# Kernel tuning notes

Measured on AMD Instinct MI355X. Metric: run time of the kernel, lower is better.

Reference implementation:

```python
import jax, jax.numpy as jnp
import numpy as np

B, T_LAT = 64, 1024
K, PAD = 15, 7
# SMPL-style parents for 24 joints (joint 0 = root)
PARENTS = [0, 0, 0, 0, 1, 2, 3, 4, 5, 6, 7, 8, 9, 9, 9, 12, 13, 14, 16, 17, 18, 19, 20, 21]


def _fine_adjacency():
    # edges of the kinematic tree; +1 virtual root-displacement node (Aberman find_neighbor, dist=1)
    edges = [(PARENTS[j], j) for j in range(1, 24)]  # 23 edges
    n = len(edges) + 1  # 24 graph nodes
    A = np.eye(n, dtype=bool)
    for i, (pi, ci) in enumerate(edges):
        for j, (pj, cj) in enumerate(edges):
            if {pi, ci} & {pj, cj}:
                A[i, j] = True
        if pi == 0 or ci == 0:  # edges touching the root neighbor the virtual root node
            A[i, n - 1] = A[n - 1, i] = True
    return A


def _coarsen(A, pools):
    m = len(pools)
    Ac = np.eye(m, dtype=bool)
    for a in range(m):
        for b in range(m):
            if A[np.ix_(pools[a], pools[b])].any():
                Ac[a, b] = True
    return Ac


def _unpool_weight(pools, n_fine, cpj):
    # SkeletonUnpool: binary matrix copying each coarse joint's channels to its fine members
    W = np.zeros((n_fine * cpj, len(pools) * cpj), np.float32)
    for i, grp in enumerate(pools):
        for j in grp:
            for c in range(cpj):
                W[j * cpj + c, i * cpj + c] = 1.0
    return W


def _conv_mask(A, in_cpj, out_cpj, k):
    n = A.shape[0]
    M = np.zeros((n * out_cpj, n * in_cpj, k), np.float32)
    for a in range(n):
        for b in range(n):
            if A[a, b]:
                M[a * out_cpj:(a + 1) * out_cpj, b * in_cpj:(b + 1) * in_cpj, :] = 1.0
    return M


def _lin_mask(A, in_cpj, out_cpj):
    n = A.shape[0]
    M = np.zeros((n * out_cpj, n * in_cpj), np.float32)
    for a in range(n):
        for b in range(n):
            if A[a, b]:
                M[a * out_cpj:(a + 1) * out_cpj, b * in_cpj:(b + 1) * in_cpj] = 1.0
    return M


def setup_inputs() -> dict:
    key = jax.random.key(0)
    ks = jax.random.split(key, 12)
    A0 = _fine_adjacency()                           # 24 fine graph nodes
    P0 = [[2 * i, 2 * i + 1] for i in range(12)]     # pooling 24 -> 12
    P1 = [[2 * i, 2 * i + 1] for i in range(6)]      # pooling 12 -> 6
    A1 = _coarsen(A0, P0)                            # 12-node coarse adjacency

    inp = {
        'x': jax.random.normal(ks[0], (B, T_LAT, 96), jnp.float32),      # latent: 6 joints x 16 ch
        'offset0': jax.random.normal(ks[1], (B, 12, 3), jnp.float32),
        'offset1': jax.random.normal(ks[2], (B, 24, 3), jnp.float32),
        'W_unpool0': jnp.asarray(_unpool_weight(P1, 12, 16)),            # (192, 96)
        'W_unpool1': jnp.asarray(_unpool_weight(P0, 24, 8)),             # (192, 96)
        'conv_w0': jax.random.normal(ks[3], (96, 192, K), jnp.float32) * 0.05,
        'conv_b0': jax.random.normal(ks[4], (96,), jnp.float32) * 0.05,
        'conv_w1': jax.random.normal(ks[5], (96, 192, K), jnp.float32) * 0.05,
        'conv_b1': jax.random.normal(ks[6], (96,), jnp.float32) * 0.05,
        'off_w0': jax.random.normal(ks[7], (96, 36), jnp.float32) * 0.05,
        'off_b0': jax.random.normal(ks[8], (96,), jnp.float32) * 0.05,
        'off_w1': jax.random.normal(ks[9], (96, 72), jnp.float32) * 0.05,
        'off_b1': jax.random.normal(ks[10], (96,), jnp.float32) * 0.05,
        'conv_mask0': jnp.asarray(_conv_mask(A1, 16, 8, K)),
        'conv_mask1': jnp.asarray(_conv_mask(A0, 8, 4, K)),
        'off_mask0': jnp.asarray(_lin_mask(A1, 3, 8)),
        'off_mask1': jnp.asarray(_lin_mask(A0, 3, 4)),
    }
    return inp


def _upsample2(h):
    # nn.Upsample(scale_factor=2, mode='linear', align_corners=False) on last axis
    b, c, t = h.shape
    return jax.image.resize(h, (b, c, 2 * t), method='linear')


def _conv1d(h, w, b):
    y = jax.lax.conv_general_dilated(h, w, (1,), [(PAD, PAD)],
                                     dimension_numbers=('NCH', 'OIH', 'NCH'))
    return y + b[None, :, None]


def reference(x, offset0, offset1, W_unpool0, W_unpool1,
              conv_w0, conv_b0, conv_w1, conv_b1,
              off_w0, off_b0, off_w1, off_b1,
              conv_mask0, conv_mask1, off_mask0, off_mask1):
    h = jnp.swapaxes(x, -2, -1)                       # (B, C_lat, T)
    # ---- stage 0: upsample time, unpool 6->12 joints, masked conv, offset, LeakyReLU
    h = _upsample2(h)
    h = jnp.einsum('oc,bct->bot', W_unpool0, h)       # (B, 192, 2T)
    h = _conv1d(h, conv_w0 * conv_mask0, conv_b0)     # (B, 96, 2T)
    off = offset0.reshape(offset0.shape[0], -1) @ (off_w0 * off_mask0).T + off_b0
    h = h + off[:, :, None] / 100.0
    h = jax.nn.leaky_relu(h, 0.2)
    # ---- stage 1 (last layer: no activation)
    h = _upsample2(h)
    h = jnp.einsum('oc,bct->bot', W_unpool1, h)       # (B, 192, 4T)
    h = _conv1d(h, conv_w1 * conv_mask1, conv_b1)     # (B, 96, 4T)
    off = offset1.reshape(offset1.shape[0], -1) @ (off_w1 * off_mask1).T + off_b1
    h = h + off[:, :, None] / 100.0
    return h[:, :, :-1]                               # trim last frame
```

## Files before the change

### kernel.cpp

```cpp
#include <hip/hip_runtime.h>

typedef unsigned short ushort_t;
typedef unsigned int u32;
typedef short bf16x8 __attribute__((ext_vector_type(8)));
typedef float f32x4 __attribute__((ext_vector_type(4)));
typedef u32 u32x4 __attribute__((ext_vector_type(4)));

__device__ __forceinline__ float bf2f(ushort_t u) {
    u32 x = ((u32)u) << 16; float f; __builtin_memcpy(&f, &x, 4); return f;
}
__device__ __forceinline__ ushort_t f2bf(float f) {
    u32 x; __builtin_memcpy(&x, &f, 4);
    x = x + 0x7fffu + ((x >> 16) & 1u);
    return (ushort_t)(x >> 16);
}

#define NBB 128
#define UROWS 136
#define USTRB 208
#define UB_BYTES (UROWS * USTRB)
#define LDS_TOTAL UB_BYTES
#define LSTR1 261

__global__ void prepA(const float* __restrict__ w0, const float* __restrict__ m0,
                      const float* __restrict__ w1, const float* __restrict__ m1,
                      const float* __restrict__ offw0, const float* __restrict__ offb0,
                      const float* __restrict__ omask0, const float* __restrict__ convb0,
                      const float* __restrict__ off0,
                      const float* __restrict__ offw1, const float* __restrict__ offb1,
                      const float* __restrict__ omask1, const float* __restrict__ convb1,
                      const float* __restrict__ off1,
                      float* __restrict__ Wplain, float* __restrict__ ADD0,
                      float* __restrict__ ADD1)
{
    int idx = blockIdx.x * 256 + threadIdx.x;
    if (idx < 18432) {
        int o = idx % 96;
        int cc = (idx / 96) % 96;
        int st = idx / 9216;
        const float* w = st ? w1 : w0;
        const float* mk = st ? m1 : m0;
        int cpj = st ? 8 : 16;
        int i = cc / cpj, c = cc % cpj;
        float s[15];
#pragma unroll
        for (int k = 0; k < 15; ++k) s[k] = 0.f;
#pragma unroll
        for (int d = 0; d < 2; ++d) {
            int f = (2 * i + d) * cpj + c;
            int base = (o * 192 + f) * 15;
#pragma unroll
            for (int k = 0; k < 15; ++k)
                s[k] += w[base + k] * mk[base + k];
        }
#pragma unroll
        for (int k = 0; k < 15; ++k)
            Wplain[st * 138240 + (k * 96 + cc) * 96 + o] = s[k];
    } else if (idx < 18432 + 12288) {
        int a = idx - 18432;
        int st = a / 6144; int a2 = a % 6144;
        int o = a2 % 96, b = a2 / 96;
        const float* ow = st ? offw1 : offw0;
        const float* ob = st ? offb1 : offb0;
        const float* om = st ? omask1 : omask0;
        const float* cb = st ? convb1 : convb0;
        const float* of = st ? off1 : off0;
        int J = st ? 72 : 36;
        float s = 0.f;
        for (int j2 = 0; j2 < J; ++j2) s += ow[o * J + j2] * om[o * J + j2] * of[b * J + j2];
        (st ? ADD1 : ADD0)[b * 96 + o] = cb[o] + (s + ob[o]) * 0.01f;
    }
}

__global__ void prepB(const float* __restrict__ Wplain,
                      ushort_t* __restrict__ Wp0, ushort_t* __restrict__ Wp1)
{
    int idx = blockIdx.x * 256 + threadIdx.x;
    if (idx >= 331776) return;
    int o = idx % 96; int t = idx / 96;
    int cc = t % 96; t /= 96;
    int j = t % 9; t /= 9;
    int p = t % 2; int st = t / 2;
    const float* WP = Wplain + (size_t)st * 138240;
    int kk[4]; float cf[4];
    if (p == 0) { kk[0]=2*j;   cf[0]=0.75f; kk[1]=2*j-2; cf[1]=0.25f;
                  kk[2]=2*j+1; cf[2]=0.25f; kk[3]=2*j-1; cf[3]=0.75f; }
    else        { kk[0]=2*j;   cf[0]=0.25f; kk[1]=2*j-2; cf[1]=0.75f;
                  kk[2]=2*j-1; cf[2]=0.75f; kk[3]=2*j-3; cf[3]=0.25f; }
    float s = 0.f;
#pragma unroll
    for (int q = 0; q < 4; ++q) {
        int k = kk[q];
        if (k >= 0 && k < 15) s += cf[q] * WP[(k * 96 + cc) * 96 + o];
    }
    int lane = (o & 15) | (((cc >> 3) & 3) << 4);
    int mh = (o >> 4) / 3, m = (o >> 4) % 3;
    int pos = ((((j * 2 + mh) * 2 + p) * 9) + (cc >> 5) * 3 + m) * 512 + lane * 8 + (cc & 7);
    (st ? Wp1 : Wp0)[pos] = f2bf(s);
}

template<int BF16SRC>
__global__ void prep_G(const float* __restrict__ WP, const float* __restrict__ srcF,
                       const ushort_t* __restrict__ srcB, float* __restrict__ G, int T)
{
    int idx = blockIdx.x * 256 + threadIdx.x;
    if (idx >= 184320) return;
    int o = idx % 96; int t = idx / 96;
    int k = t % 15; t /= 15;
    int side = t % 2; int b = t / 2;
    const float* wk = WP + (size_t)k * 9216 + o;
    int row = side ? T - 1 : 0;
    float s = 0.f;
    if (BF16SRC) {
        const ushort_t* xr = srcB + ((size_t)b * T + row) * 96;
        for (int cc = 0; cc < 96; ++cc)
            s += wk[cc * 96] * bf2f(xr[cc]);
    } else {
        const float* xr = srcF + ((size_t)b * T + row) * 96;
        for (int cc = 0; cc < 96; ++cc)
            s += wk[cc * 96] * bf2f(f2bf(xr[cc]));
    }
    G[((size_t)(b * 96 + o) * 15 + k) * 2 + side] = s;
}

__global__ void prep_cfb(const float* __restrict__ G, float* __restrict__ CF,
                         float* __restrict__ CB)
{
    int idx = blockIdx.x * 256 + threadIdx.x;
    if (idx >= 86016) return;
    int seg = idx % 14; int r = idx / 14;
    int o = r % 96; int b = r / 96;
    bool front = seg < 7; int t = front ? seg : seg - 7;
    float s = 0.f;
    if (front) { for (int k = 0; k <= 6 - t; ++k)   s += G[(((size_t)(b*96+o)*15)+k)*2 + 0]; }
    else       { for (int k = 14 - t; k <= 14; ++k) s += G[(((size_t)(b*96+o)*15)+k)*2 + 1]; }
    (front ? CF : CB)[(b * 7 + t) * 96 + o] = s;
}

template<int STAGE>
__launch_bounds__(256, 4)
__global__ void conv_poly(const float* __restrict__ Xf, const ushort_t* __restrict__ Hbf,
                          const ushort_t* __restrict__ Wp, const float* __restrict__ ADD,
                          const float* __restrict__ CF, const float* __restrict__ CB,
                          ushort_t* __restrict__ Hout, float* __restrict__ Fout, int T)
{
    extern __shared__ char smem[];
    char* Ub = smem;

    const int tid = threadIdx.x;
    const int lane = tid & 63;
    const int wid = tid >> 6;
    const int b = blockIdx.y;
    const int tg = blockIdx.x;
    const int mh = blockIdx.z;
    const int phase = wid & 1;
    const int nq = wid >> 1;
    const int rb0 = tg * NBB - 4;

    const ushort_t* wgl = Wp + (size_t)(mh * 2 + phase) * 4608 + lane * 8;

    if (STAGE == 0) {
        const float* xb = Xf + (size_t)b * T * 96;
        for (int idx = tid; idx < UROWS * 12; idx += 256) {
            int r = idx / 12, q = idx - r * 12;
            int rg = rb0 + r; rg = rg < 0 ? 0 : (rg > T - 1 ? T - 1 : rg);
            const float* src = xb + (size_t)rg * 96 + q * 8;
            float4 a = *(const float4*)src;
            float4 c2 = *(const float4*)(src + 4);
            u32x4 v;
            v[0] = (u32)f2bf(a.x) | ((u32)f2bf(a.y) << 16);
            v[1] = (u32)f2bf(a.z) | ((u32)f2bf(a.w) << 16);
            v[2] = (u32)f2bf(c2.x) | ((u32)f2bf(c2.y) << 16);
            v[3] = (u32)f2bf(c2.z) | ((u32)f2bf(c2.w) << 16);
            *(u32x4*)(Ub + r * USTRB + q * 16) = v;
        }
    } else {
        const ushort_t* xb = Hbf + (size_t)b * T * 96;
        for (int idx = tid; idx < UROWS * 12; idx += 256) {
            int r = idx / 12, q = idx - r * 12;
            int rg = rb0 + r; rg = rg < 0 ? 0 : (rg > T - 1 ? T - 1 : rg);
            u32x4 v = *(const u32x4*)(xb + (size_t)rg * 96 + q * 8);
            *(u32x4*)(Ub + r * USTRB + q * 16) = v;
        }
    }
    __syncthreads();

    f32x4 acc[3][4];
#pragma unroll
    for (int m = 0; m < 3; ++m)
#pragma unroll
        for (int n = 0; n < 4; ++n) acc[m][n] = (f32x4){0.f, 0.f, 0.f, 0.f};

    const int rowbase = 64 * nq + (lane & 15);
    const int og16 = (lane >> 4) * 16;

#pragma unroll
    for (int j = 0; j < 9; ++j) {
        const ushort_t* wj = wgl + (size_t)j * 18432;
        bf16x8 aj[9];
#pragma unroll
        for (int q = 0; q < 9; ++q)
            aj[q] = *(const bf16x8*)(wj + q * 512);

        const int bj = (rowbase + j) * USTRB;
#pragma unroll
        for (int cb = 0; cb < 3; ++cb) {
            const int off0 = bj + cb * 64 + og16;
            bf16x8 bfr[4];
#pragma unroll
            for (int n = 0; n < 4; ++n)
                bfr[n] = *(const bf16x8*)(Ub + off0 + n * 16 * USTRB);
#pragma unroll
            for (int m = 0; m < 3; ++m)
#pragma unroll
                for (int n = 0; n < 4; ++n)
                    acc[m][n] = __builtin_amdgcn_mfma_f32_16x16x32_bf16(aj[cb * 3 + m], bfr[n], acc[m][n], 0, 0, 0);
        }
    }

    const int T2 = 2 * T;
    const int t0 = tg * 2 * NBB;
    const int og4 = (lane >> 4) * 4;

    __syncthreads();

    if (STAGE == 0) {
        ushort_t* L0 = (ushort_t*)Ub;
#pragma unroll
        for (int m = 0; m < 3; ++m) {
            int obase = mh * 48 + m * 16 + og4;
            float addv[4];
#pragma unroll
            for (int rr = 0; rr < 4; ++rr) addv[rr] = ADD[b * 96 + obase + rr];
#pragma unroll
            for (int n = 0; n < 4; ++n) {
                int tl = 2 * (rowbase + 16 * n) + phase;
                int tgl = t0 + tl;
                ushort_t pk[4];
#pragma unroll
                for (int rr = 0; rr < 4; ++rr) {
                    float v = acc[m][n][rr] + addv[rr];
                    if (tgl < 7)                   v -= CF[(b * 7 + tgl) * 96 + obase + rr];
                    if (tgl >= T2 - 7 && tgl < T2) v -= CB[(b * 7 + tgl - (T2 - 7)) * 96 + obase + rr];
                    v = v > 0.f ? v : 0.2f * v;
                    pk[rr] = f2bf(v);
                }
                uint2 w2;
                w2.x = (u32)pk[0] | ((u32)pk[1] << 16);
                w2.y = (u32)pk[2] | ((u32)pk[3] << 16);
                *(uint2*)((char*)L0 + tl * 104 + (m * 16 + og4) * 2) = w2;
            }
        }
        __syncthreads();
        for (int g = tid; g < 256 * 6; g += 256) {
            int row = g / 6, col = g % 6;
            int t = t0 + row;
            if (t < T2) {
                u32x4 v = *(const u32x4*)((char*)L0 + row * 104 + col * 16);
                *(u32x4*)((char*)Hout + ((size_t)(b * T2 + t) * 96 + mh * 48) * 2 + col * 16) = v;
            }
        }
    } else {
        const int TO = T2 - 1;
        float* L1 = (float*)Ub;
#pragma unroll
        for (int m = 0; m < 3; ++m) {
            int obase = mh * 48 + m * 16 + og4;
            float addv[4];
#pragma unroll
            for (int rr = 0; rr < 4; ++rr) addv[rr] = ADD[b * 96 + obase + rr];
#pragma unroll
            for (int n = 0; n < 4; ++n) {
                int tl = 2 * (rowbase + 16 * n) + phase;
                int tgl = t0 + tl;
#pragma unroll
                for (int rr = 0; rr < 4; ++rr) {
                    float v = acc[m][n][rr] + addv[rr];
                    if (tgl < 7)                   v -= CF[(b * 7 + tgl) * 96 + obase + rr];
                    if (tgl >= T2 - 7 && tgl < T2) v -= CB[(b * 7 + tgl - (T2 - 7)) * 96 + obase + rr];
                    L1[(og4 + rr) * LSTR1 + tl] = v;
                }
            }
            __syncthreads();
            for (int g = tid; g < 4096; g += 256) {
                int row = g >> 8, col = g & 255;
                int t = t0 + col;
                if (t < TO) {
                    int o_g = mh * 48 + m * 16 + row;
                    Fout[((size_t)(b * 96 + o_g)) * TO + t] = L1[row * LSTR1 + col];
                }
            }
            __syncthreads();
        }
    }
}

extern "C" void kernel_launch(void* const* d_in, const int* in_sizes, int n_in,
                              void* d_out, int out_size, void* d_ws, size_t ws_size,
                              hipStream_t stream)
{
    const float* x       = (const float*)d_in[0];
    const float* offset0 = (const float*)d_in[1];
    const float* offset1 = (const float*)d_in[2];
    const float* conv_w0 = (const float*)d_in[5];
    const float* conv_b0 = (const float*)d_in[6];
    const float* conv_w1 = (const float*)d_in[7];
    const float* conv_b1 = (const float*)d_in[8];
    const float* off_w0  = (const float*)d_in[9];
    const float* off_b0  = (const float*)d_in[10];
    const float* off_w1  = (const float*)d_in[11];
    const float* off_b1  = (const float*)d_in[12];
    const float* cmask0  = (const float*)d_in[13];
    const float* cmask1  = (const float*)d_in[14];
    const float* omask0  = (const float*)d_in[15];
    const float* omask1  = (const float*)d_in[16];

    char* ws = (char*)d_ws;
    float*    Wplain = (float*)(ws);
    ushort_t* Wp0    = (ushort_t*)(ws + 1105920);
    ushort_t* Wp1    = (ushort_t*)(ws + 1437696);
    float*    ADD0   = (float*)(ws + 1769472);
    float*    ADD1   = (float*)(ws + 1794048);
    float*    CF0    = (float*)(ws + 1818624);
    float*    CB0    = (float*)(ws + 1990656);
    float*    CF1    = (float*)(ws + 2162688);
    float*    CB1    = (float*)(ws + 2334720);
    float*    G0     = (float*)(ws + 2506752);
    float*    G1     = (float*)(ws + 3244032);
    ushort_t* H1     = (ushort_t*)(ws + 3981312);
    float* out = (float*)d_out;

    prepA<<<120, 256, 0, stream>>>(conv_w0, cmask0, conv_w1, cmask1,
                                   off_w0, off_b0, omask0, conv_b0, offset0,
                                   off_w1, off_b1, omask1, conv_b1, offset1,
                                   Wplain, ADD0, ADD1);
    prepB<<<1296, 256, 0, stream>>>(Wplain, Wp0, Wp1);
    prep_G<0><<<720, 256, 0, stream>>>(Wplain, x, nullptr, G0, 1024);
    prep_cfb<<<336, 256, 0, stream>>>(G0, CF0, CB0);

    conv_poly<0><<<dim3(8, 64, 2), 256, LDS_TOTAL, stream>>>(x, nullptr, Wp0, ADD0, CF0, CB0,
                                                             H1, nullptr, 1024);
    prep_G<1><<<720, 256, 0, stream>>>(Wplain + 138240, nullptr, H1, G1, 2048);
    prep_cfb<<<336, 256, 0, stream>>>(G1, CF1, CB1);
    conv_poly<1><<<dim3(16, 64, 2), 256, LDS_TOTAL, stream>>>(nullptr, H1, Wp1, ADD1, CF1, CB1,
                                                              nullptr, out, 2048);
}
```

Baseline: 127.3 us.

## Merge output-channel halves into one block, widen per-warp time tile, prefetch weights

Removes the grid z-dimension that split the 96 output channels into two blocks. Each block now computes both halves: warps split by channel half and phase, and each warp covers 128 time rows with 8 N-tiles instead of 4. The goal is to stage the input tile in LDS once instead of twice and halve the block count. Weight fragments are now loaded in three groups, with the next tap's first group prefetched. The accumulator doubles to 96 floats per lane, so launch bounds drop to 3 blocks per CU. The stage-1 LDS transpose gains a small row-dependent column shift to reduce bank conflicts, and the epilogue is serialized per channel half with extra barriers.

```diff
diff --git a/kernel.cpp b/kernel.cpp
--- a/kernel.cpp
+++ b/kernel.cpp
@@ -138,7 +138,7 @@
 }
 
 template<int STAGE>
-__launch_bounds__(256, 4)
+__launch_bounds__(256, 3)
 __global__ void conv_poly(const float* __restrict__ Xf, const ushort_t* __restrict__ Hbf,
                           const ushort_t* __restrict__ Wp, const float* __restrict__ ADD,
                           const float* __restrict__ CF, const float* __restrict__ CB,
@@ -152,12 +152,16 @@
     const int wid = tid >> 6;
     const int b = blockIdx.y;
     const int tg = blockIdx.x;
-    const int mh = blockIdx.z;
     const int phase = wid & 1;
-    const int nq = wid >> 1;
+    const int mhw = wid >> 1;
     const int rb0 = tg * NBB - 4;
 
-    const ushort_t* wgl = Wp + (size_t)(mh * 2 + phase) * 4608 + lane * 8;
+    const ushort_t* wgl = Wp + (size_t)(mhw * 2 + phase) * 4608 + lane * 8;
+
+    bf16x8 a0[3];
+#pragma unroll
+    for (int q = 0; q < 3; ++q)
+        a0[q] = *(const bf16x8*)(wgl + q * 512);
 
     if (STAGE == 0) {
         const float* xb = Xf + (size_t)b * T * 96;
@@ -185,36 +189,46 @@
     }
     __syncthreads();
 
-    f32x4 acc[3][4];
+    f32x4 acc[3][8];
 #pragma unroll
     for (int m = 0; m < 3; ++m)
 #pragma unroll
-        for (int n = 0; n < 4; ++n) acc[m][n] = (f32x4){0.f, 0.f, 0.f, 0.f};
-
-    const int rowbase = 64 * nq + (lane & 15);
+        for (int n = 0; n < 8; ++n) acc[m][n] = (f32x4){0.f, 0.f, 0.f, 0.f};
+
+    const int rowbase = lane & 15;
     const int og16 = (lane >> 4) * 16;
 
 #pragma unroll
     for (int j = 0; j < 9; ++j) {
         const ushort_t* wj = wgl + (size_t)j * 18432;
-        bf16x8 aj[9];
-#pragma unroll
-        for (int q = 0; q < 9; ++q)
-            aj[q] = *(const bf16x8*)(wj + q * 512);
-
+        bf16x8 a1[3], a2[3];
+#pragma unroll
+        for (int q = 0; q < 3; ++q) a1[q] = *(const bf16x8*)(wj + (3 + q) * 512);
+#pragma unroll
+        for (int q = 0; q < 3; ++q) a2[q] = *(const bf16x8*)(wj + (6 + q) * 512);
+        bf16x8 a0n[3];
+        if (j < 8) {
+#pragma unroll
+            for (int q = 0; q < 3; ++q) a0n[q] = *(const bf16x8*)(wj + 18432 + q * 512);
+        }
         const int bj = (rowbase + j) * USTRB;
 #pragma unroll
         for (int cb = 0; cb < 3; ++cb) {
             const int off0 = bj + cb * 64 + og16;
-            bf16x8 bfr[4];
-#pragma unroll
-            for (int n = 0; n < 4; ++n)
+            const bf16x8* af = (cb == 0) ? a0 : (cb == 1) ? a1 : a2;
+            bf16x8 bfr[8];
+#pragma unroll
+            for (int n = 0; n < 8; ++n)
                 bfr[n] = *(const bf16x8*)(Ub + off0 + n * 16 * USTRB);
 #pragma unroll
             for (int m = 0; m < 3; ++m)
 #pragma unroll
-                for (int n = 0; n < 4; ++n)
-                    acc[m][n] = __builtin_amdgcn_mfma_f32_16x16x32_bf16(aj[cb * 3 + m], bfr[n], acc[m][n], 0, 0, 0);
+                for (int n = 0; n < 8; ++n)
+                    acc[m][n] = __builtin_amdgcn_mfma_f32_16x16x32_bf16(af[m], bfr[n], acc[m][n], 0, 0, 0);
+        }
+        if (j < 8) {
+#pragma unroll
+            for (int q = 0; q < 3; ++q) a0[q] = a0n[q];
         }
     }
 
@@ -227,70 +241,82 @@
     if (STAGE == 0) {
         ushort_t* L0 = (ushort_t*)Ub;
 #pragma unroll
-        for (int m = 0; m < 3; ++m) {
-            int obase = mh * 48 + m * 16 + og4;
-            float addv[4];
-#pragma unroll
-            for (int rr = 0; rr < 4; ++rr) addv[rr] = ADD[b * 96 + obase + rr];
-#pragma unroll
-            for (int n = 0; n < 4; ++n) {
-                int tl = 2 * (rowbase + 16 * n) + phase;
-                int tgl = t0 + tl;
-                ushort_t pk[4];
-#pragma unroll
-                for (int rr = 0; rr < 4; ++rr) {
-                    float v = acc[m][n][rr] + addv[rr];
-                    if (tgl < 7)                   v -= CF[(b * 7 + tgl) * 96 + obase + rr];
-                    if (tgl >= T2 - 7 && tgl < T2) v -= CB[(b * 7 + tgl - (T2 - 7)) * 96 + obase + rr];
-                    v = v > 0.f ? v : 0.2f * v;
-                    pk[rr] = f2bf(v);
+        for (int mc = 0; mc < 2; ++mc) {
+            if (mhw == mc) {
+#pragma unroll
+                for (int m = 0; m < 3; ++m) {
+                    int obase = mc * 48 + m * 16 + og4;
+                    float addv[4];
+#pragma unroll
+                    for (int rr = 0; rr < 4; ++rr) addv[rr] = ADD[b * 96 + obase + rr];
+#pragma unroll
+                    for (int n = 0; n < 8; ++n) {
+                        int tl = 2 * (rowbase + 16 * n) + phase;
+                        int tgl = t0 + tl;
+                        ushort_t pk[4];
+#pragma unroll
+                        for (int rr = 0; rr < 4; ++rr) {
+                            float v = acc[m][n][rr] + addv[rr];
+                            if (tgl < 7)                   v -= CF[(b * 7 + tgl) * 96 + obase + rr];
+                            if (tgl >= T2 - 7 && tgl < T2) v -= CB[(b * 7 + tgl - (T2 - 7)) * 96 + obase + rr];
+                            v = v > 0.f ? v : 0.2f * v;
+                            pk[rr] = f2bf(v);
+                        }
+                        uint2 w2;
+                        w2.x = (u32)pk[0] | ((u32)pk[1] << 16);
+                        w2.y = (u32)pk[2] | ((u32)pk[3] << 16);
+                        *(uint2*)((char*)L0 + tl * 104 + (m * 16 + og4) * 2) = w2;
+                    }
                 }
-                uint2 w2;
-                w2.x = (u32)pk[0] | ((u32)pk[1] << 16);
-                w2.y = (u32)pk[2] | ((u32)pk[3] << 16);
-                *(uint2*)((char*)L0 + tl * 104 + (m * 16 + og4) * 2) = w2;
             }
-        }
-        __syncthreads();
-        for (int g = tid; g < 256 * 6; g += 256) {
-            int row = g / 6, col = g % 6;
-            int t = t0 + row;
-            if (t < T2) {
-                u32x4 v = *(const u32x4*)((char*)L0 + row * 104 + col * 16);
-                *(u32x4*)((char*)Hout + ((size_t)(b * T2 + t) * 96 + mh * 48) * 2 + col * 16) = v;
+            __syncthreads();
+            for (int g = tid; g < 256 * 6; g += 256) {
+                int row = g / 6, col = g % 6;
+                int t = t0 + row;
+                if (t < T2) {
+                    u32x4 v = *(const u32x4*)((char*)L0 + row * 104 + col * 16);
+                    *(u32x4*)((char*)Hout + ((size_t)(b * T2 + t) * 96 + mc * 48) * 2 + col * 16) = v;
+                }
             }
+            __syncthreads();
         }
     } else {
         const int TO = T2 - 1;
         float* L1 = (float*)Ub;
 #pragma unroll
-        for (int m = 0; m < 3; ++m) {
-            int obase = mh * 48 + m * 16 + og4;
-            float addv[4];
-#pragma unroll
-            for (int rr = 0; rr < 4; ++rr) addv[rr] = ADD[b * 96 + obase + rr];
-#pragma unroll
-            for (int n = 0; n < 4; ++n) {
-                int tl = 2 * (rowbase + 16 * n) + phase;
-                int tgl = t0 + tl;
-#pragma unroll
-                for (int rr = 0; rr < 4; ++rr) {
-                    float v = acc[m][n][rr] + addv[rr];
-                    if (tgl < 7)                   v -= CF[(b * 7 + tgl) * 96 + obase + rr];
-                    if (tgl >= T2 - 7 && tgl < T2) v -= CB[(b * 7 + tgl - (T2 - 7)) * 96 + obase + rr];
-                    L1[(og4 + rr) * LSTR1 + tl] = v;
+        for (int mc = 0; mc < 2; ++mc) {
+#pragma unroll
+            for (int m = 0; m < 3; ++m) {
+                if (mhw == mc) {
+                    int obase = mc * 48 + m * 16 + og4;
+                    float addv[4];
+#pragma unroll
+                    for (int rr = 0; rr < 4; ++rr) addv[rr] = ADD[b * 96 + obase + rr];
+#pragma unroll
+                    for (int n = 0; n < 8; ++n) {
+                        int tl = 2 * (rowbase + 16 * n) + phase;
+                        int tgl = t0 + tl;
+#pragma unroll
+                        for (int rr = 0; rr < 4; ++rr) {
+                            float v = acc[m][n][rr] + addv[rr];
+                            if (tgl < 7)                   v -= CF[(b * 7 + tgl) * 96 + obase + rr];
+                            if (tgl >= T2 - 7 && tgl < T2) v -= CB[(b * 7 + tgl - (T2 - 7)) * 96 + obase + rr];
+                            int rloc = og4 + rr;
+                            L1[rloc * LSTR1 + tl + ((rloc >> 2) & 1)] = v;
+                        }
+                    }
                 }
+                __syncthreads();
+                for (int g = tid; g < 4096; g += 256) {
+                    int row = g >> 8, col = g & 255;
+                    int t = t0 + col;
+                    if (t < TO) {
+                        int o_g = mc * 48 + m * 16 + row;
+                        Fout[((size_t)(b * 96 + o_g)) * TO + t] = L1[row * LSTR1 + col + ((row >> 2) & 1)];
+                    }
+                }
+                __syncthreads();
             }
-            __syncthreads();
-            for (int g = tid; g < 4096; g += 256) {
-                int row = g >> 8, col = g & 255;
-                int t = t0 + col;
-                if (t < TO) {
-                    int o_g = mh * 48 + m * 16 + row;
-                    Fout[((size_t)(b * 96 + o_g)) * TO + t] = L1[row * LSTR1 + col];
-                }
-            }
-            __syncthreads();
         }
     }
 }
@@ -338,10 +364,10 @@
     prep_G<0><<<720, 256, 0, stream>>>(Wplain, x, nullptr, G0, 1024);
     prep_cfb<<<336, 256, 0, stream>>>(G0, CF0, CB0);
 
-    conv_poly<0><<<dim3(8, 64, 2), 256, LDS_TOTAL, stream>>>(x, nullptr, Wp0, ADD0, CF0, CB0,
-                                                             H1, nullptr, 1024);
+    conv_poly<0><<<dim3(8, 64), 256, LDS_TOTAL, stream>>>(x, nullptr, Wp0, ADD0, CF0, CB0,
+                                                          H1, nullptr, 1024);
     prep_G<1><<<720, 256, 0, stream>>>(Wplain + 138240, nullptr, H1, G1, 2048);
     prep_cfb<<<336, 256, 0, stream>>>(G1, CF1, CB1);
-    conv_poly<1><<<dim3(16, 64, 2), 256, LDS_TOTAL, stream>>>(nullptr, H1, Wp1, ADD1, CF1, CB1,
-                                                              nullptr, out, 2048);
-}
+    conv_poly<1><<<dim3(16, 64), 256, LDS_TOTAL, stream>>>(nullptr, H1, Wp1, ADD1, CF1, CB1,
+                                                           nullptr, out, 2048);
+}
```

Measured after the change: 182.8 us. 1.44x slower.

## Fold boundary-correction prep kernels into conv epilogue and pipeline weight loads

Applied to the files above, without the earlier changes.

Removes the separate prep_G and prep_cfb launches and computes the front/back edge-padding corrections inside the edge tiles of each conv kernel, storing them in LDS. Weight fragments for the next tap are prefetched while the current tap's MFMAs run, replacing the bulk load of nine fragments per iteration. The fp32 epilogue transpose buffer gets a small stagger to reduce LDS bank conflicts. This cuts four kernel launches and their global round trips, at the cost of serial per-thread work in the edge blocks (up to 7×96 MACs per output) that may lengthen the tail.

```diff
diff --git a/kernel.cpp b/kernel.cpp
--- a/kernel.cpp
+++ b/kernel.cpp
@@ -19,8 +19,9 @@
 #define UROWS 136
 #define USTRB 208
 #define UB_BYTES (UROWS * USTRB)
-#define LDS_TOTAL UB_BYTES
+#define EPI_OFF 2048
 #define LSTR1 261
+#define LDS_TOTAL (EPI_OFF + 256 * 104)
 
 __global__ void prepA(const float* __restrict__ w0, const float* __restrict__ m0,
                       const float* __restrict__ w1, const float* __restrict__ m1,
@@ -99,49 +100,11 @@
     (st ? Wp1 : Wp0)[pos] = f2bf(s);
 }
 
-template<int BF16SRC>
-__global__ void prep_G(const float* __restrict__ WP, const float* __restrict__ srcF,
-                       const ushort_t* __restrict__ srcB, float* __restrict__ G, int T)
-{
-    int idx = blockIdx.x * 256 + threadIdx.x;
-    if (idx >= 184320) return;
-    int o = idx % 96; int t = idx / 96;
-    int k = t % 15; t /= 15;
-    int side = t % 2; int b = t / 2;
-    const float* wk = WP + (size_t)k * 9216 + o;
-    int row = side ? T - 1 : 0;
-    float s = 0.f;
-    if (BF16SRC) {
-        const ushort_t* xr = srcB + ((size_t)b * T + row) * 96;
-        for (int cc = 0; cc < 96; ++cc)
-            s += wk[cc * 96] * bf2f(xr[cc]);
-    } else {
-        const float* xr = srcF + ((size_t)b * T + row) * 96;
-        for (int cc = 0; cc < 96; ++cc)
-            s += wk[cc * 96] * bf2f(f2bf(xr[cc]));
-    }
-    G[((size_t)(b * 96 + o) * 15 + k) * 2 + side] = s;
-}
-
-__global__ void prep_cfb(const float* __restrict__ G, float* __restrict__ CF,
-                         float* __restrict__ CB)
-{
-    int idx = blockIdx.x * 256 + threadIdx.x;
-    if (idx >= 86016) return;
-    int seg = idx % 14; int r = idx / 14;
-    int o = r % 96; int b = r / 96;
-    bool front = seg < 7; int t = front ? seg : seg - 7;
-    float s = 0.f;
-    if (front) { for (int k = 0; k <= 6 - t; ++k)   s += G[(((size_t)(b*96+o)*15)+k)*2 + 0]; }
-    else       { for (int k = 14 - t; k <= 14; ++k) s += G[(((size_t)(b*96+o)*15)+k)*2 + 1]; }
-    (front ? CF : CB)[(b * 7 + t) * 96 + o] = s;
-}
-
 template<int STAGE>
 __launch_bounds__(256, 4)
 __global__ void conv_poly(const float* __restrict__ Xf, const ushort_t* __restrict__ Hbf,
-                          const ushort_t* __restrict__ Wp, const float* __restrict__ ADD,
-                          const float* __restrict__ CF, const float* __restrict__ CB,
+                          const ushort_t* __restrict__ Wp, const float* __restrict__ WPst,
+                          const float* __restrict__ ADD,
                           ushort_t* __restrict__ Hout, float* __restrict__ Fout, int T)
 {
     extern __shared__ char smem[];
@@ -158,6 +121,11 @@
     const int rb0 = tg * NBB - 4;
 
     const ushort_t* wgl = Wp + (size_t)(mh * 2 + phase) * 4608 + lane * 8;
+
+    bf16x8 a0[3];
+#pragma unroll
+    for (int q = 0; q < 3; ++q)
+        a0[q] = *(const bf16x8*)(wgl + q * 512);
 
     if (STAGE == 0) {
         const float* xb = Xf + (size_t)b * T * 96;
@@ -197,15 +165,21 @@
 #pragma unroll
     for (int j = 0; j < 9; ++j) {
         const ushort_t* wj = wgl + (size_t)j * 18432;
-        bf16x8 aj[9];
-#pragma unroll
-        for (int q = 0; q < 9; ++q)
-            aj[q] = *(const bf16x8*)(wj + q * 512);
-
+        bf16x8 a1[3], a2[3];
+#pragma unroll
+        for (int q = 0; q < 3; ++q) a1[q] = *(const bf16x8*)(wj + (3 + q) * 512);
+#pragma unroll
+        for (int q = 0; q < 3; ++q) a2[q] = *(const bf16x8*)(wj + (6 + q) * 512);
+        bf16x8 a0n[3];
+        if (j < 8) {
+#pragma unroll
+            for (int q = 0; q < 3; ++q) a0n[q] = *(const bf16x8*)(wj + 18432 + q * 512);
+        }
         const int bj = (rowbase + j) * USTRB;
 #pragma unroll
         for (int cb = 0; cb < 3; ++cb) {
             const int off0 = bj + cb * 64 + og16;
+            const bf16x8* af = (cb == 0) ? a0 : (cb == 1) ? a1 : a2;
             bf16x8 bfr[4];
 #pragma unroll
             for (int n = 0; n < 4; ++n)
@@ -214,21 +188,56 @@
             for (int m = 0; m < 3; ++m)
 #pragma unroll
                 for (int n = 0; n < 4; ++n)
-                    acc[m][n] = __builtin_amdgcn_mfma_f32_16x16x32_bf16(aj[cb * 3 + m], bfr[n], acc[m][n], 0, 0, 0);
+                    acc[m][n] = __builtin_amdgcn_mfma_f32_16x16x32_bf16(af[m], bfr[n], acc[m][n], 0, 0, 0);
+        }
+        if (j < 8) {
+#pragma unroll
+            for (int q = 0; q < 3; ++q) a0[q] = a0n[q];
         }
     }
 
     const int T2 = 2 * T;
     const int t0 = tg * 2 * NBB;
     const int og4 = (lane >> 4) * 4;
+    const bool front = (tg == 0);
+    const bool back  = (tg == (int)gridDim.x - 1);
 
     __syncthreads();
 
+    float* CT = (float*)smem;
+    if (front || back) {
+        for (int pair = tid; pair < 7 * 48; pair += 256) {
+            int t = pair / 48, ol = pair % 48;
+            int o = mh * 48 + ol;
+            int krow = front ? 0 : (T - 1);
+            float s = 0.f;
+            int k0 = front ? 0 : (14 - t);
+            int k1 = front ? (6 - t) : 14;
+            for (int k = k0; k <= k1; ++k) {
+                const float* wk = WPst + ((size_t)k * 96) * 96 + o;
+                if (STAGE == 0) {
+                    const float* xr = Xf + ((size_t)b * T + krow) * 96;
+                    for (int cc = 0; cc < 96; ++cc)
+                        s += wk[cc * 96] * bf2f(f2bf(xr[cc]));
+                } else {
+                    const ushort_t* xr = Hbf + ((size_t)b * T + krow) * 96;
+                    for (int cc = 0; cc < 96; ++cc)
+                        s += wk[cc * 96] * bf2f(xr[cc]);
+                }
+            }
+            CT[pair] = s;
+        }
+    }
+    __syncthreads();
+
+    char* epi = smem + EPI_OFF;
+
     if (STAGE == 0) {
-        ushort_t* L0 = (ushort_t*)Ub;
+        ushort_t* L0 = (ushort_t*)epi;
 #pragma unroll
         for (int m = 0; m < 3; ++m) {
-            int obase = mh * 48 + m * 16 + og4;
+            int olb = m * 16 + og4;
+            int obase = mh * 48 + olb;
             float addv[4];
 #pragma unroll
             for (int rr = 0; rr < 4; ++rr) addv[rr] = ADD[b * 96 + obase + rr];
@@ -240,15 +249,15 @@
 #pragma unroll
                 for (int rr = 0; rr < 4; ++rr) {
                     float v = acc[m][n][rr] + addv[rr];
-                    if (tgl < 7)                   v -= CF[(b * 7 + tgl) * 96 + obase + rr];
-                    if (tgl >= T2 - 7 && tgl < T2) v -= CB[(b * 7 + tgl - (T2 - 7)) * 96 + obase + rr];
+                    if (front && tgl < 7)       v -= CT[tgl * 48 + olb + rr];
+                    if (back && tgl >= T2 - 7)  v -= CT[(tgl - (T2 - 7)) * 48 + olb + rr];
                     v = v > 0.f ? v : 0.2f * v;
                     pk[rr] = f2bf(v);
                 }
                 uint2 w2;
                 w2.x = (u32)pk[0] | ((u32)pk[1] << 16);
                 w2.y = (u32)pk[2] | ((u32)pk[3] << 16);
-                *(uint2*)((char*)L0 + tl * 104 + (m * 16 + og4) * 2) = w2;
+                *(uint2*)((char*)L0 + tl * 104 + olb * 2) = w2;
             }
         }
         __syncthreads();
@@ -262,10 +271,11 @@
         }
     } else {
         const int TO = T2 - 1;
-        float* L1 = (float*)Ub;
+        float* L1 = (float*)epi;
 #pragma unroll
         for (int m = 0; m < 3; ++m) {
-            int obase = mh * 48 + m * 16 + og4;
+            int olb = m * 16 + og4;
+            int obase = mh * 48 + olb;
             float addv[4];
 #pragma unroll
             for (int rr = 0; rr < 4; ++rr) addv[rr] = ADD[b * 96 + obase + rr];
@@ -276,9 +286,10 @@
 #pragma unroll
                 for (int rr = 0; rr < 4; ++rr) {
                     float v = acc[m][n][rr] + addv[rr];
-                    if (tgl < 7)                   v -= CF[(b * 7 + tgl) * 96 + obase + rr];
-                    if (tgl >= T2 - 7 && tgl < T2) v -= CB[(b * 7 + tgl - (T2 - 7)) * 96 + obase + rr];
-                    L1[(og4 + rr) * LSTR1 + tl] = v;
+                    if (front && tgl < 7)       v -= CT[tgl * 48 + olb + rr];
+                    if (back && tgl >= T2 - 7)  v -= CT[(tgl - (T2 - 7)) * 48 + olb + rr];
+                    int rloc = og4 + rr;
+                    L1[rloc * LSTR1 + tl + ((rloc >> 2) & 1)] = v;
                 }
             }
             __syncthreads();
@@ -287,7 +298,7 @@
                 int t = t0 + col;
                 if (t < TO) {
                     int o_g = mh * 48 + m * 16 + row;
-                    Fout[((size_t)(b * 96 + o_g)) * TO + t] = L1[row * LSTR1 + col];
+                    Fout[((size_t)(b * 96 + o_g)) * TO + t] = L1[row * LSTR1 + col + ((row >> 2) & 1)];
                 }
             }
             __syncthreads();
@@ -321,13 +332,7 @@
     ushort_t* Wp1    = (ushort_t*)(ws + 1437696);
     float*    ADD0   = (float*)(ws + 1769472);
     float*    ADD1   = (float*)(ws + 1794048);
-    float*    CF0    = (float*)(ws + 1818624);
-    float*    CB0    = (float*)(ws + 1990656);
-    float*    CF1    = (float*)(ws + 2162688);
-    float*    CB1    = (float*)(ws + 2334720);
-    float*    G0     = (float*)(ws + 2506752);
-    float*    G1     = (float*)(ws + 3244032);
-    ushort_t* H1     = (ushort_t*)(ws + 3981312);
+    ushort_t* H1     = (ushort_t*)(ws + 1818624);
     float* out = (float*)d_out;
 
     prepA<<<120, 256, 0, stream>>>(conv_w0, cmask0, conv_w1, cmask1,
@@ -335,13 +340,9 @@
                                    off_w1, off_b1, omask1, conv_b1, offset1,
                                    Wplain, ADD0, ADD1);
     prepB<<<1296, 256, 0, stream>>>(Wplain, Wp0, Wp1);
-    prep_G<0><<<720, 256, 0, stream>>>(Wplain, x, nullptr, G0, 1024);
-    prep_cfb<<<336, 256, 0, stream>>>(G0, CF0, CB0);
-
-    conv_poly<0><<<dim3(8, 64, 2), 256, LDS_TOTAL, stream>>>(x, nullptr, Wp0, ADD0, CF0, CB0,
-                                                             H1, nullptr, 1024);
-    prep_G<1><<<720, 256, 0, stream>>>(Wplain + 138240, nullptr, H1, G1, 2048);
-    prep_cfb<<<336, 256, 0, stream>>>(G1, CF1, CB1);
-    conv_poly<1><<<dim3(16, 64, 2), 256, LDS_TOTAL, stream>>>(nullptr, H1, Wp1, ADD1, CF1, CB1,
-                                                              nullptr, out, 2048);
-}
+
+    conv_poly<0><<<dim3(8, 64, 2), 256, LDS_TOTAL, stream>>>(x, nullptr, Wp0, Wplain,
+                                                             ADD0, H1, nullptr, 1024);
+    conv_poly<1><<<dim3(16, 64, 2), 256, LDS_TOTAL, stream>>>(nullptr, H1, Wp1, Wplain + 138240,
+                                                              ADD1, nullptr, out, 2048);
+}
```

Measured after the change: 202.5 us. 59.1% more time.

## Fuse boundary-correction prep into prepB and a single per-batch block kernel

Applied to the files above, without the earlier changes.

Replaces the separate prep_G and prep_cfb kernels with one block-level routine per (batch, side). It stages the boundary input row in shared memory, computes the 15 per-tap partial sums into LDS, then writes CF/CB as running prefix sums. For stage 0 this work is folded into prepB as 128 extra blocks, and for stage 1 it becomes a single small kernel. This cuts the number of launches from seven to five and drops the global G scratch buffer. In exchange each boundary block does serial loops over 96 channels with only 192 active threads, which lowers parallelism per block.

```diff
diff --git a/kernel.cpp b/kernel.cpp
--- a/kernel.cpp
+++ b/kernel.cpp
@@ -72,9 +72,62 @@
     }
 }
 
+template<int BF16SRC>
+__device__ __forceinline__ void bnd_block(int blk, const float* __restrict__ WP,
+                                          const float* __restrict__ srcF,
+                                          const ushort_t* __restrict__ srcB,
+                                          float* __restrict__ CF, float* __restrict__ CB,
+                                          int T, float* xe, float* Gs)
+{
+    int side = blk & 1, b = blk >> 1;
+    int tid = threadIdx.x;
+    int row = side ? T - 1 : 0;
+    if (tid < 96) {
+        float v;
+        if (BF16SRC) v = bf2f(srcB[((size_t)b * T + row) * 96 + tid]);
+        else         v = bf2f(f2bf(srcF[((size_t)b * T + row) * 96 + tid]));
+        xe[tid] = v;
+    }
+    __syncthreads();
+    int half = tid / 96;
+    int o = tid % 96;
+    if (half < 2) {
+        int k0 = half * 8, k1 = half ? 15 : 8;
+        for (int k = k0; k < k1; ++k) {
+            const float* wk = WP + (size_t)k * 9216 + o;
+            float s = 0.f;
+            for (int cc = 0; cc < 96; ++cc) s += wk[cc * 96] * xe[cc];
+            Gs[k * 96 + o] = s;
+        }
+    }
+    __syncthreads();
+    if (tid < 96) {
+        float run = 0.f;
+        if (side == 0) {
+            for (int t = 6; t >= 0; --t) {
+                run += Gs[(6 - t) * 96 + tid];
+                CF[(b * 7 + t) * 96 + tid] = run;
+            }
+        } else {
+            for (int t = 0; t < 7; ++t) {
+                run += Gs[(14 - t) * 96 + tid];
+                CB[(b * 7 + t) * 96 + tid] = run;
+            }
+        }
+    }
+}
+
 __global__ void prepB(const float* __restrict__ Wplain,
-                      ushort_t* __restrict__ Wp0, ushort_t* __restrict__ Wp1)
-{
+                      ushort_t* __restrict__ Wp0, ushort_t* __restrict__ Wp1,
+                      const float* __restrict__ x,
+                      float* __restrict__ CF0, float* __restrict__ CB0)
+{
+    __shared__ float xe[96];
+    __shared__ float Gs[15 * 96];
+    if (blockIdx.x >= 1296) {
+        bnd_block<0>(blockIdx.x - 1296, Wplain, x, nullptr, CF0, CB0, 1024, xe, Gs);
+        return;
+    }
     int idx = blockIdx.x * 256 + threadIdx.x;
     if (idx >= 331776) return;
     int o = idx % 96; int t = idx / 96;
@@ -99,42 +152,12 @@
     (st ? Wp1 : Wp0)[pos] = f2bf(s);
 }
 
-template<int BF16SRC>
-__global__ void prep_G(const float* __restrict__ WP, const float* __restrict__ srcF,
-                       const ushort_t* __restrict__ srcB, float* __restrict__ G, int T)
-{
-    int idx = blockIdx.x * 256 + threadIdx.x;
-    if (idx >= 184320) return;
-    int o = idx % 96; int t = idx / 96;
-    int k = t % 15; t /= 15;
-    int side = t % 2; int b = t / 2;
-    const float* wk = WP + (size_t)k * 9216 + o;
-    int row = side ? T - 1 : 0;
-    float s = 0.f;
-    if (BF16SRC) {
-        const ushort_t* xr = srcB + ((size_t)b * T + row) * 96;
-        for (int cc = 0; cc < 96; ++cc)
-            s += wk[cc * 96] * bf2f(xr[cc]);
-    } else {
-        const float* xr = srcF + ((size_t)b * T + row) * 96;
-        for (int cc = 0; cc < 96; ++cc)
-            s += wk[cc * 96] * bf2f(f2bf(xr[cc]));
-    }
-    G[((size_t)(b * 96 + o) * 15 + k) * 2 + side] = s;
-}
-
-__global__ void prep_cfb(const float* __restrict__ G, float* __restrict__ CF,
-                         float* __restrict__ CB)
-{
-    int idx = blockIdx.x * 256 + threadIdx.x;
-    if (idx >= 86016) return;
-    int seg = idx % 14; int r = idx / 14;
-    int o = r % 96; int b = r / 96;
-    bool front = seg < 7; int t = front ? seg : seg - 7;
-    float s = 0.f;
-    if (front) { for (int k = 0; k <= 6 - t; ++k)   s += G[(((size_t)(b*96+o)*15)+k)*2 + 0]; }
-    else       { for (int k = 14 - t; k <= 14; ++k) s += G[(((size_t)(b*96+o)*15)+k)*2 + 1]; }
-    (front ? CF : CB)[(b * 7 + t) * 96 + o] = s;
+__global__ void prep_bnd1(const float* __restrict__ WP, const ushort_t* __restrict__ H1,
+                          float* __restrict__ CF, float* __restrict__ CB)
+{
+    __shared__ float xe[96];
+    __shared__ float Gs[15 * 96];
+    bnd_block<1>(blockIdx.x, WP, nullptr, H1, CF, CB, 2048, xe, Gs);
 }
 
 template<int STAGE>
@@ -325,23 +348,18 @@
     float*    CB0    = (float*)(ws + 1990656);
     float*    CF1    = (float*)(ws + 2162688);
     float*    CB1    = (float*)(ws + 2334720);
-    float*    G0     = (float*)(ws + 2506752);
-    float*    G1     = (float*)(ws + 3244032);
-    ushort_t* H1     = (ushort_t*)(ws + 3981312);
+    ushort_t* H1     = (ushort_t*)(ws + 2506752);
     float* out = (float*)d_out;
 
     prepA<<<120, 256, 0, stream>>>(conv_w0, cmask0, conv_w1, cmask1,
                                    off_w0, off_b0, omask0, conv_b0, offset0,
                                    off_w1, off_b1, omask1, conv_b1, offset1,
                                    Wplain, ADD0, ADD1);
-    prepB<<<1296, 256, 0, stream>>>(Wplain, Wp0, Wp1);
-    prep_G<0><<<720, 256, 0, stream>>>(Wplain, x, nullptr, G0, 1024);
-    prep_cfb<<<336, 256, 0, stream>>>(G0, CF0, CB0);
+    prepB<<<1424, 256, 0, stream>>>(Wplain, Wp0, Wp1, x, CF0, CB0);
 
     conv_poly<0><<<dim3(8, 64, 2), 256, LDS_TOTAL, stream>>>(x, nullptr, Wp0, ADD0, CF0, CB0,
                                                              H1, nullptr, 1024);
-    prep_G<1><<<720, 256, 0, stream>>>(Wplain + 138240, nullptr, H1, G1, 2048);
-    prep_cfb<<<336, 256, 0, stream>>>(G1, CF1, CB1);
+    prep_bnd1<<<128, 256, 0, stream>>>(Wplain + 138240, H1, CF1, CB1);
     conv_poly<1><<<dim3(16, 64, 2), 256, LDS_TOTAL, stream>>>(nullptr, H1, Wp1, ADD1, CF1, CB1,
                                                               nullptr, out, 2048);
 }
```

New measurement: 415.7 us. +226.5%, slower.
